# Kernel tuning notes

Measured on AMD Instinct MI355X. Metric: run time of the kernel, lower is better.

The kernel has to match this reference:

```python
import jax, jax.numpy as jnp
import numpy as np

N, DIM = 131072, 512

def setup_inputs() -> dict:
    key = jax.random.key(0)
    k1, k2, k3 = jax.random.split(key, 3)
    x = jax.random.normal(k1, (N, DIM), dtype=jnp.float32)
    mask = jax.random.bernoulli(k2, 0.5, (N,))
    # xavier_uniform for square [dim, dim]: bound = sqrt(6/(dim+dim))
    bound = float(np.sqrt(6.0 / (DIM + DIM)))
    deletion_weight = jax.random.uniform(k3, (DIM, DIM), dtype=jnp.float32,
                                         minval=-bound, maxval=bound)
    return {"x": x, "mask": mask, "deletion_weight": deletion_weight}

def reference(x, mask, deletion_weight):
    # new_rep = x.clone(); new_rep[mask] = new_rep[mask] @ W
    # Equivalent dense form: rows where mask -> x @ W, else unchanged.
    transformed = jnp.matmul(x, deletion_weight)  # [N, dim]
    return jnp.where(mask[:, None], transformed, x)
```

## Files before the change

### kernel.cpp

```cpp
#include <hip/hip_runtime.h>
#include <hip/hip_bf16.h>

#define DIMK 512
#define NROWS 131072

typedef __bf16 bf16x8 __attribute__((ext_vector_type(8)));
typedef float f32x4 __attribute__((ext_vector_type(4)));

__device__ __attribute__((aligned(16))) unsigned short g_Wt2[DIMK * DIMK];
__device__ __attribute__((aligned(16))) unsigned short g_A[(size_t)NROWS * DIMK];
__device__ int g_rows[NROWS];
__device__ int g_cnt[1];

static __device__ __forceinline__ void gload_lds16(const unsigned short* g, unsigned short* l) {
    __builtin_amdgcn_global_load_lds(
        (const __attribute__((address_space(1))) void*)(unsigned long)(g),
        (__attribute__((address_space(3))) void*)(unsigned long)(l), 16, 0, 0);
}

static __device__ __forceinline__ unsigned short f2bf(float f) {
    unsigned u = __builtin_bit_cast(unsigned, f);
    u += 0x7FFFu + ((u >> 16) & 1u);
    return (unsigned short)(u >> 16);
}

__global__ void wprep_kernel(const float* __restrict__ W) {
    if (blockIdx.x == 0 && threadIdx.x == 0) g_cnt[0] = 0;
    __shared__ float tile[64][65];
    const int bk = blockIdx.x & 7;
    const int bn = blockIdx.x >> 3;
    const int t = threadIdx.x;
    const int rl = t >> 2;
    const int ch = t & 3;

    const float* src = W + (bk * 64 + rl) * DIMK + bn * 64 + ch * 16;
    float4 v[4];
#pragma unroll
    for (int i = 0; i < 4; i++) v[i] = reinterpret_cast<const float4*>(src)[i];
#pragma unroll
    for (int i = 0; i < 4; i++) {
        tile[rl][ch * 16 + i * 4 + 0] = v[i].x;
        tile[rl][ch * 16 + i * 4 + 1] = v[i].y;
        tile[rl][ch * 16 + i * 4 + 2] = v[i].z;
        tile[rl][ch * 16 + i * 4 + 3] = v[i].w;
    }
    __syncthreads();

    unsigned short o[16];
#pragma unroll
    for (int i = 0; i < 16; i++) o[i] = f2bf(tile[ch * 16 + i][rl]);
    const int nblk = bn * 4 + (rl >> 4);
    const int kchunk = bk * 8 + ch * 2;
    unsigned short* dst = g_Wt2 + nblk * 8192 + kchunk * 128 + (rl & 15) * 8;
    *reinterpret_cast<uint4*>(dst) = *reinterpret_cast<uint4*>(&o[0]);
    *reinterpret_cast<uint4*>(dst + 128) = *reinterpret_cast<uint4*>(&o[8]);
}

__global__ __launch_bounds__(256)
void prep_kernel(const float* __restrict__ X, const void* __restrict__ maskp,
                 float* __restrict__ out) {
    __shared__ int s_flags;
    __shared__ int s_pos[64];
    const int b = blockIdx.x;
    const int t = threadIdx.x;
    if (t == 0) s_flags = 0;
    __syncthreads();
    {
        unsigned w = ((const unsigned*)maskp)[(b & 127) * 256 + t];
        int fl = (w > 1u) ? 1 : 0;
        if ((t & 1) && w != 0u) fl |= 2;
        if (fl) atomicOr(&s_flags, fl);
    }
    __syncthreads();
    const int fl = s_flags;
    const int md = (fl & 1) ? 0 : ((fl & 2) ? 1 : 2);

    if (t < 64) {
        const int row = b * 64 + t;
        bool pred;
        if (md == 0)      pred = ((const unsigned char*)maskp)[row] != 0;
        else if (md == 1) pred = ((const int*)maskp)[row] != 0;
        else              pred = ((const unsigned*)maskp)[2l * row] != 0;
        unsigned long long bal = __ballot(pred);
        int pre = __popcll(bal & ((1ull << t) - 1ull));
        int cnt = __popcll(bal);
        int base = 0;
        if (t == 0 && cnt) base = atomicAdd(&g_cnt[0], cnt);
        base = __shfl(base, 0);
        const int pos = base + pre;
        if (pred) g_rows[pos] = row;
        s_pos[t] = pred ? pos : -1;
    }
    __syncthreads();

    const int wid = t >> 6;
    const int lane = t & 63;
    const long r0 = (long)b * 64 + wid * 16;

    int pos16[16];
#pragma unroll
    for (int i = 0; i < 16; i++) pos16[i] = s_pos[wid * 16 + i];

#pragma unroll
    for (int ii = 0; ii < 16; ii += 8) {
        f32x4 v[8][2];
#pragma unroll
        for (int j = 0; j < 8; j++) {
            const f32x4* src = reinterpret_cast<const f32x4*>(X + (r0 + ii + j) * DIMK);
            v[j][0] = __builtin_nontemporal_load(&src[2 * lane]);
            v[j][1] = __builtin_nontemporal_load(&src[2 * lane + 1]);
        }
#pragma unroll
        for (int j = 0; j < 8; j++) {
            const int p = pos16[ii + j];
            if (p >= 0) {
                unsigned short o[8];
                o[0] = f2bf(v[j][0][0]); o[1] = f2bf(v[j][0][1]);
                o[2] = f2bf(v[j][0][2]); o[3] = f2bf(v[j][0][3]);
                o[4] = f2bf(v[j][1][0]); o[5] = f2bf(v[j][1][1]);
                o[6] = f2bf(v[j][1][2]); o[7] = f2bf(v[j][1][3]);
                *reinterpret_cast<uint4*>(g_A + (long)p * DIMK + lane * 8) =
                    *reinterpret_cast<uint4*>(&o[0]);
            } else {
                f32x4* d = reinterpret_cast<f32x4*>(out + (r0 + ii + j) * DIMK);
                __builtin_nontemporal_store(v[j][0], &d[2 * lane]);
                __builtin_nontemporal_store(v[j][1], &d[2 * lane + 1]);
            }
        }
    }
}

__global__ __launch_bounds__(512)
void gemm_kernel(float* __restrict__ out) {
    __shared__ __attribute__((aligned(16))) unsigned short Als[8192];
    __shared__ __attribute__((aligned(16))) unsigned short Bls[16384];

    const int nmask = g_cnt[0];
    const int x = blockIdx.x & 7;
    const int q = blockIdx.x >> 3;
    const int tm = (q >> 1) * 8 + x;
    const int tn = q & 1;
    if (tm * 128 >= nmask) return;

    const int t = threadIdx.x;
    const int lane = t & 63;
    const int wid = t >> 6;
    const int wr = wid >> 2, wc = wid & 3;
    const int l15 = lane & 15, lhi = lane >> 4;

    const unsigned short* asrc[2];
#pragma unroll
    for (int i = 0; i < 2; i++)
        asrc[i] = g_A + ((long)(tm * 8 + wid) * 16 + (lane & 15)) * DIMK
                      + (i * 4 + (lane >> 4)) * 8;
    const unsigned short* bsrc = g_Wt2 + ((long)tn * 16 + wid * 2) * 8192 + lane * 8;
    unsigned short* adst = Als + wid * 1024;
    unsigned short* bdst = Bls + (wid * 2) * 1024;

    f32x4 acc[4][4] = {};

    const unsigned aro = (wr * 4) * 1024 + lhi * 128 + l15 * 8;
    const unsigned bro = (wc * 4) * 1024 + lhi * 128 + l15 * 8;

#pragma unroll 1
    for (int kt = 0; kt < 8; kt++) {
#pragma unroll
        for (int i = 0; i < 2; i++) {
            gload_lds16(asrc[i] + kt * 64, adst + i * 512);
#pragma unroll
            for (int g = 0; g < 2; g++)
                gload_lds16(bsrc + g * 8192 + kt * 1024 + i * 512,
                            bdst + g * 1024 + i * 512);
        }
        __syncthreads();

#pragma unroll
        for (int s = 0; s < 2; s++) {
            bf16x8 afr[4], bfr[4];
#pragma unroll
            for (int m = 0; m < 4; m++)
                afr[m] = *reinterpret_cast<const bf16x8*>(Als + aro + m * 1024 + s * 512);
#pragma unroll
            for (int n = 0; n < 4; n++)
                bfr[n] = *reinterpret_cast<const bf16x8*>(Bls + bro + n * 1024 + s * 512);
#pragma unroll
            for (int m = 0; m < 4; m++)
#pragma unroll
                for (int n = 0; n < 4; n++)
                    acc[m][n] = __builtin_amdgcn_mfma_f32_16x16x32_bf16(
                        afr[m], bfr[n], acc[m][n], 0, 0, 0);
        }
        __syncthreads();
    }

    const int colb = tn * 256 + wc * 64;
#pragma unroll
    for (int m = 0; m < 4; m++) {
        const int rl_ = wr * 64 + m * 16 + lhi * 4;
#pragma unroll
        for (int j = 0; j < 4; j++) {
            const int pos = tm * 128 + rl_ + j;
            if (pos < nmask) {
                const long rg = g_rows[pos];
                float* orow = out + rg * DIMK + colb;
#pragma unroll
                for (int n = 0; n < 4; n++)
                    orow[n * 16 + l15] = acc[m][n][j];
            }
        }
    }
}

extern "C" void kernel_launch(void* const* d_in, const int* in_sizes, int n_in,
                              void* d_out, int out_size, void* d_ws, size_t ws_size,
                              hipStream_t stream) {
    const float* X = (const float*)d_in[0];
    const void* mask = d_in[1];
    const float* W = (const float*)d_in[2];
    float* out = (float*)d_out;

    hipLaunchKernelGGL(wprep_kernel, dim3(64), dim3(256), 0, stream, W);
    hipLaunchKernelGGL(prep_kernel, dim3(NROWS / 64), dim3(256), 0, stream, X, mask, out);
    hipLaunchKernelGGL(gemm_kernel, dim3(2048), dim3(512), 0, stream, out);
}
```

Measured before the change: 157.8 us.

## Gather fp32 rows directly in GEMM, drop bf16 staging buffer

```diff
diff --git a/kernel.cpp b/kernel.cpp
--- a/kernel.cpp
+++ b/kernel.cpp
@@ -8,11 +8,10 @@
 typedef float f32x4 __attribute__((ext_vector_type(4)));
 
 __device__ __attribute__((aligned(16))) unsigned short g_Wt2[DIMK * DIMK];
-__device__ __attribute__((aligned(16))) unsigned short g_A[(size_t)NROWS * DIMK];
 __device__ int g_rows[NROWS];
-__device__ int g_cnt[1];
-
-static __device__ __forceinline__ void gload_lds16(const unsigned short* g, unsigned short* l) {
+__device__ int g_cnt[2];
+
+static __device__ __forceinline__ void gload_lds16(const void* g, void* l) {
     __builtin_amdgcn_global_load_lds(
         (const __attribute__((address_space(1))) void*)(unsigned long)(g),
         (__attribute__((address_space(3))) void*)(unsigned long)(l), 16, 0, 0);
@@ -24,8 +23,10 @@
     return (unsigned short)(u >> 16);
 }
 
+static __device__ __forceinline__ int swz32(int s) { return (s ^ (s >> 3)) & 31; }
+
 __global__ void wprep_kernel(const float* __restrict__ W) {
-    if (blockIdx.x == 0 && threadIdx.x == 0) g_cnt[0] = 0;
+    if (blockIdx.x == 0 && threadIdx.x == 0) { g_cnt[0] = 0; g_cnt[1] = 0; }
     __shared__ float tile[64][65];
     const int bk = blockIdx.x & 7;
     const int bn = blockIdx.x >> 3;
@@ -56,11 +57,8 @@
     *reinterpret_cast<uint4*>(dst + 128) = *reinterpret_cast<uint4*>(&o[8]);
 }
 
-__global__ __launch_bounds__(256)
-void prep_kernel(const float* __restrict__ X, const void* __restrict__ maskp,
-                 float* __restrict__ out) {
+__global__ void partition_kernel(const void* __restrict__ maskp) {
     __shared__ int s_flags;
-    __shared__ int s_pos[64];
     const int b = blockIdx.x;
     const int t = threadIdx.x;
     if (t == 0) s_flags = 0;
@@ -75,54 +73,58 @@
     const int fl = s_flags;
     const int md = (fl & 1) ? 0 : ((fl & 2) ? 1 : 2);
 
-    if (t < 64) {
-        const int row = b * 64 + t;
-        bool pred;
-        if (md == 0)      pred = ((const unsigned char*)maskp)[row] != 0;
-        else if (md == 1) pred = ((const int*)maskp)[row] != 0;
-        else              pred = ((const unsigned*)maskp)[2l * row] != 0;
-        unsigned long long bal = __ballot(pred);
-        int pre = __popcll(bal & ((1ull << t) - 1ull));
-        int cnt = __popcll(bal);
-        int base = 0;
-        if (t == 0 && cnt) base = atomicAdd(&g_cnt[0], cnt);
-        base = __shfl(base, 0);
-        const int pos = base + pre;
-        if (pred) g_rows[pos] = row;
-        s_pos[t] = pred ? pos : -1;
-    }
-    __syncthreads();
-
-    const int wid = t >> 6;
+    const int row = b * 256 + t;
+    bool pred;
+    if (md == 0)      pred = ((const unsigned char*)maskp)[row] != 0;
+    else if (md == 1) pred = ((const int*)maskp)[row] != 0;
+    else              pred = ((const unsigned*)maskp)[2l * row] != 0;
+
     const int lane = t & 63;
-    const long r0 = (long)b * 64 + wid * 16;
-
-    int pos16[16];
-#pragma unroll
-    for (int i = 0; i < 16; i++) pos16[i] = s_pos[wid * 16 + i];
+    unsigned long long bal = __ballot(pred);
+    int pre = __popcll(bal & ((1ull << lane) - 1ull));
+    int cnt = __popcll(bal);
+    int base = 0;
+    if (lane == 0 && cnt) base = atomicAdd(&g_cnt[0], cnt);
+    base = __shfl(base, 0);
+    if (pred) g_rows[base + pre] = row;
+    int base2 = 0;
+    if (lane == 0 && cnt < 64) base2 = atomicAdd(&g_cnt[1], 64 - cnt);
+    base2 = __shfl(base2, 0);
+    if (!pred) g_rows[NROWS - 1 - (base2 + (lane - pre))] = row;
+}
+
+__global__ __launch_bounds__(256)
+void prep_kernel(const float* __restrict__ X, float* __restrict__ out) {
+    const int ncopy = g_cnt[1];
+    const int bid = blockIdx.x;
+    if (bid * 64 >= ncopy) return;
+    const int wid = threadIdx.x >> 6;
+    const int lane = threadIdx.x & 63;
+    const int base = bid * 64 + wid * 16;
+
+    long rows[16];
+    unsigned vmask = 0;
+#pragma unroll
+    for (int i = 0; i < 16; i++) {
+        const int pos = base + i;
+        const bool ok = pos < ncopy;
+        rows[i] = g_rows[NROWS - 1 - (ok ? pos : 0)];
+        vmask |= (ok ? 1u : 0u) << i;
+    }
 
 #pragma unroll
     for (int ii = 0; ii < 16; ii += 8) {
         f32x4 v[8][2];
 #pragma unroll
         for (int j = 0; j < 8; j++) {
-            const f32x4* src = reinterpret_cast<const f32x4*>(X + (r0 + ii + j) * DIMK);
+            const f32x4* src = reinterpret_cast<const f32x4*>(X + rows[ii + j] * DIMK);
             v[j][0] = __builtin_nontemporal_load(&src[2 * lane]);
             v[j][1] = __builtin_nontemporal_load(&src[2 * lane + 1]);
         }
 #pragma unroll
         for (int j = 0; j < 8; j++) {
-            const int p = pos16[ii + j];
-            if (p >= 0) {
-                unsigned short o[8];
-                o[0] = f2bf(v[j][0][0]); o[1] = f2bf(v[j][0][1]);
-                o[2] = f2bf(v[j][0][2]); o[3] = f2bf(v[j][0][3]);
-                o[4] = f2bf(v[j][1][0]); o[5] = f2bf(v[j][1][1]);
-                o[6] = f2bf(v[j][1][2]); o[7] = f2bf(v[j][1][3]);
-                *reinterpret_cast<uint4*>(g_A + (long)p * DIMK + lane * 8) =
-                    *reinterpret_cast<uint4*>(&o[0]);
-            } else {
-                f32x4* d = reinterpret_cast<f32x4*>(out + (r0 + ii + j) * DIMK);
+            if ((vmask >> (ii + j)) & 1u) {
+                f32x4* d = reinterpret_cast<f32x4*>(out + rows[ii + j] * DIMK);
                 __builtin_nontemporal_store(v[j][0], &d[2 * lane]);
                 __builtin_nontemporal_store(v[j][1], &d[2 * lane + 1]);
             }
@@ -131,9 +133,10 @@
 }
 
 __global__ __launch_bounds__(512)
-void gemm_kernel(float* __restrict__ out) {
-    __shared__ __attribute__((aligned(16))) unsigned short Als[8192];
+void gemm_kernel(const float* __restrict__ X, float* __restrict__ out) {
+    __shared__ __attribute__((aligned(16))) float Als[8192];
     __shared__ __attribute__((aligned(16))) unsigned short Bls[16384];
+    __shared__ int rlist[128];
 
     const int nmask = g_cnt[0];
     const int x = blockIdx.x & 7;
@@ -148,47 +151,60 @@
     const int wr = wid >> 2, wc = wid & 3;
     const int l15 = lane & 15, lhi = lane >> 4;
 
-    const unsigned short* asrc[2];
-#pragma unroll
-    for (int i = 0; i < 2; i++)
-        asrc[i] = g_A + ((long)(tm * 8 + wid) * 16 + (lane & 15)) * DIMK
-                      + (i * 4 + (lane >> 4)) * 8;
+    if (t < 128) {
+        const int pos = tm * 128 + t;
+        rlist[t] = g_rows[pos < nmask ? pos : 0];
+    }
+    __syncthreads();
+
+    const int s_log = swz32(lane & 31);
+    const long arow = rlist[wid * 16 + (s_log >> 1)];
+    const float* abase = X + arow * DIMK + (s_log & 1) * 4 + (lane >> 5) * 8;
+    float* adst = Als + wid * 1024;
+
     const unsigned short* bsrc = g_Wt2 + ((long)tn * 16 + wid * 2) * 8192 + lane * 8;
-    unsigned short* adst = Als + wid * 1024;
     unsigned short* bdst = Bls + (wid * 2) * 1024;
 
     f32x4 acc[4][4] = {};
-
-    const unsigned aro = (wr * 4) * 1024 + lhi * 128 + l15 * 8;
+    const unsigned pu = swz32(2 * l15) * 4;
+    const unsigned pv = swz32(2 * l15 + 1) * 4;
+    const unsigned aroc = lhi * 128;
     const unsigned bro = (wc * 4) * 1024 + lhi * 128 + l15 * 8;
 
 #pragma unroll 1
     for (int kt = 0; kt < 8; kt++) {
 #pragma unroll
-        for (int i = 0; i < 2; i++) {
-            gload_lds16(asrc[i] + kt * 64, adst + i * 512);
-#pragma unroll
-            for (int g = 0; g < 2; g++)
+        for (int i = 0; i < 4; i++)
+            gload_lds16(abase + kt * 64 + i * 16, adst + i * 256);
+#pragma unroll
+        for (int g = 0; g < 2; g++)
+#pragma unroll
+            for (int i = 0; i < 2; i++)
                 gload_lds16(bsrc + g * 8192 + kt * 1024 + i * 512,
                             bdst + g * 1024 + i * 512);
-        }
         __syncthreads();
 
 #pragma unroll
         for (int s = 0; s < 2; s++) {
-            bf16x8 afr[4], bfr[4];
-#pragma unroll
-            for (int m = 0; m < 4; m++)
-                afr[m] = *reinterpret_cast<const bf16x8*>(Als + aro + m * 1024 + s * 512);
+            bf16x8 bfr[4];
 #pragma unroll
             for (int n = 0; n < 4; n++)
                 bfr[n] = *reinterpret_cast<const bf16x8*>(Bls + bro + n * 1024 + s * 512);
 #pragma unroll
-            for (int m = 0; m < 4; m++)
+            for (int m = 0; m < 4; m++) {
+                const float* ap = Als + (wr * 4 + m) * 1024 + s * 512 + aroc;
+                f32x4 u = *reinterpret_cast<const f32x4*>(ap + pu);
+                f32x4 v = *reinterpret_cast<const f32x4*>(ap + pv);
+                bf16x8 a;
+                a[0] = (__bf16)u[0]; a[1] = (__bf16)u[1];
+                a[2] = (__bf16)u[2]; a[3] = (__bf16)u[3];
+                a[4] = (__bf16)v[0]; a[5] = (__bf16)v[1];
+                a[6] = (__bf16)v[2]; a[7] = (__bf16)v[3];
 #pragma unroll
                 for (int n = 0; n < 4; n++)
                     acc[m][n] = __builtin_amdgcn_mfma_f32_16x16x32_bf16(
-                        afr[m], bfr[n], acc[m][n], 0, 0, 0);
+                        a, bfr[n], acc[m][n], 0, 0, 0);
+            }
         }
         __syncthreads();
     }
@@ -220,6 +236,7 @@
     float* out = (float*)d_out;
 
     hipLaunchKernelGGL(wprep_kernel, dim3(64), dim3(256), 0, stream, W);
-    hipLaunchKernelGGL(prep_kernel, dim3(NROWS / 64), dim3(256), 0, stream, X, mask, out);
-    hipLaunchKernelGGL(gemm_kernel, dim3(2048), dim3(512), 0, stream, out);
-}
+    hipLaunchKernelGGL(partition_kernel, dim3(NROWS / 256), dim3(256), 0, stream, mask);
+    hipLaunchKernelGGL(prep_kernel, dim3(2048), dim3(256), 0, stream, X, out);
+    hipLaunchKernelGGL(gemm_kernel, dim3(2048), dim3(512), 0, stream, X, out);
+}
```

Result: slower. 202.9 us (+28.6%).
